# Kernel tuning notes

Hardware: AMD Instinct MI355X
Metric: run time of the kernel (lower is better)

## Reference

```python
import jax, jax.numpy as jnp
import numpy as np

DIM = 4096
X_H_SCALE = 1.0
HAD_SCALE = 1.0 / np.sqrt(DIM)  # orthonormal FWHT normalization


def fwht(x):
    """Fast Walsh-Hadamard transform along the last axis (Sylvester order).
    x: [..., N] with N a power of 2. O(N log N) butterfly, fully vectorized
    over all leading dims; the loop is over the fixed log2(N) stages only.
    """
    n = x.shape[-1]
    stages = int(np.log2(n))
    assert 1 << stages == n, "last dim must be a power of 2"
    lead = x.shape[:-1]
    for i in range(stages):
        blk = 1 << i  # block size doubling each stage
        y = x.reshape(lead + (n // (2 * blk), 2, blk))
        a = y[..., 0, :]
        b = y[..., 1, :]
        x = jnp.concatenate([a + b, a - b], axis=-1).reshape(lead + (n,))
    return x


def setup_inputs() -> dict:
    key = jax.random.key(0)
    x = jax.random.normal(key, (4, 2048, DIM), dtype=jnp.float32)
    return {"x": x}


def reference(x):
    # forward: qx = FWHT(x) * (had_scale / x_H_scale)
    scale = jnp.asarray(HAD_SCALE / X_H_SCALE, dtype=x.dtype)
    return fwht(x) * scale
```

## Files before the change

### kernel.cpp

```cpp
#include <hip/hip_runtime.h>

#define DIM 4096
#define HAD_SCALE 0.015625f

__device__ __forceinline__ int swz(int a) {
    return a ^ (((a >> 6) & 7) << 2);
}

__device__ __forceinline__ void fwht16(float r[16]) {
#pragma unroll
    for (int s = 1; s < 16; s <<= 1) {
#pragma unroll
        for (int i = 0; i < 16; i++) {
            if ((i & s) == 0) {
                float a = r[i];
                float b = r[i ^ s];
                r[i]     = a + b;
                r[i ^ s] = a - b;
            }
        }
    }
}

__global__ __launch_bounds__(256) void fwht_kernel(const float* __restrict__ x,
                                                   float* __restrict__ y) {
    __shared__ float lds[DIM];
    const int t = threadIdx.x;
    const size_t row = blockIdx.x;
    const float* xin = x + row * DIM;
    float* yout = y + row * DIM;

    float r[16];

    const float4* __restrict__ x4 = (const float4*)xin;
#pragma unroll
    for (int c = 0; c < 4; c++) {
        float4 v = x4[c * 256 + t];
        r[4 * c + 0] = v.x;
        r[4 * c + 1] = v.y;
        r[4 * c + 2] = v.z;
        r[4 * c + 3] = v.w;
    }
    fwht16(r);

#pragma unroll
    for (int c = 0; c < 4; c++) {
        int a = swz(4 * t + 1024 * c);
        *(float4*)&lds[a] = make_float4(r[4 * c + 0], r[4 * c + 1],
                                        r[4 * c + 2], r[4 * c + 3]);
    }
    __syncthreads();

    const int baseB = (t & 3) + ((t >> 2) << 6);
#pragma unroll
    for (int m = 0; m < 16; m++) r[m] = lds[swz(baseB + (m << 2))];
    fwht16(r);
#pragma unroll
    for (int m = 0; m < 16; m++) lds[swz(baseB + (m << 2))] = r[m];
    __syncthreads();

    const int baseC = (t & 63) + ((t >> 6) << 10);
#pragma unroll
    for (int m = 0; m < 16; m++) r[m] = lds[swz(baseC + (m << 6))];
    fwht16(r);

#pragma unroll
    for (int m = 0; m < 16; m++) yout[baseC + (m << 6)] = r[m] * HAD_SCALE;
}

extern "C" void kernel_launch(void* const* d_in, const int* in_sizes, int n_in,
                              void* d_out, int out_size, void* d_ws, size_t ws_size,
                              hipStream_t stream) {
    const float* x = (const float*)d_in[0];
    float* y = (float*)d_out;
    const int n = in_sizes[0];
    const int rows = n / DIM;
    fwht_kernel<<<rows, 256, 0, stream>>>(x, y);
}
```

Before: 225.6 us.

## Use one wave per row with 64-point register FWHT and single LDS pass

Restructures the 4096-point transform so each 64-thread block does two 64-point in-register butterfly stages with a single LDS exchange, instead of three 16-point stages with two exchanges across 256 threads. This removes one LDS round trip and one barrier. In exchange, register pressure rises sharply (64 floats per thread) and the final global stores become strided 4-byte writes rather than coalesced contiguous ones, which may hurt memory efficiency and occupancy.

After: 247.5 us. 1.1x slower.

```diff
diff --git a/kernel.cpp b/kernel.cpp
--- a/kernel.cpp
+++ b/kernel.cpp
@@ -4,14 +4,14 @@
 #define HAD_SCALE 0.015625f
 
 __device__ __forceinline__ int swz(int a) {
-    return a ^ (((a >> 6) & 7) << 2);
+    return a ^ (((a >> 8) & 7) << 2);
 }
 
-__device__ __forceinline__ void fwht16(float r[16]) {
+__device__ __forceinline__ void fwht64(float* r) {
 #pragma unroll
-    for (int s = 1; s < 16; s <<= 1) {
+    for (int s = 1; s < 64; s <<= 1) {
 #pragma unroll
-        for (int i = 0; i < 16; i++) {
+        for (int i = 0; i < 64; i++) {
             if ((i & s) == 0) {
                 float a = r[i];
                 float b = r[i ^ s];
@@ -22,50 +22,62 @@
     }
 }
 
-__global__ __launch_bounds__(256) void fwht_kernel(const float* __restrict__ x,
-                                                   float* __restrict__ y) {
+__global__ __launch_bounds__(64, 4) void fwht_kernel(const float* __restrict__ x,
+                                                     float* __restrict__ y) {
     __shared__ float lds[DIM];
-    const int t = threadIdx.x;
+    const int L = threadIdx.x;
     const size_t row = blockIdx.x;
     const float* xin = x + row * DIM;
     float* yout = y + row * DIM;
 
-    float r[16];
+    float4 r4[16];
+    float* r = (float*)r4;
 
     const float4* __restrict__ x4 = (const float4*)xin;
 #pragma unroll
-    for (int c = 0; c < 4; c++) {
-        float4 v = x4[c * 256 + t];
-        r[4 * c + 0] = v.x;
-        r[4 * c + 1] = v.y;
-        r[4 * c + 2] = v.z;
-        r[4 * c + 3] = v.w;
-    }
-    fwht16(r);
+    for (int c = 0; c < 16; c++) r4[c] = x4[c * 64 + L];
 
 #pragma unroll
-    for (int c = 0; c < 4; c++) {
-        int a = swz(4 * t + 1024 * c);
-        *(float4*)&lds[a] = make_float4(r[4 * c + 0], r[4 * c + 1],
-                                        r[4 * c + 2], r[4 * c + 3]);
+    for (int c = 0; c < 16; c++) {
+        float a0 = r[4 * c + 0], a1 = r[4 * c + 1];
+        float a2 = r[4 * c + 2], a3 = r[4 * c + 3];
+        float b0 = a0 + a1, b1 = a0 - a1, b2 = a2 + a3, b3 = a2 - a3;
+        r[4 * c + 0] = b0 + b2;
+        r[4 * c + 1] = b1 + b3;
+        r[4 * c + 2] = b0 - b2;
+        r[4 * c + 3] = b1 - b3;
+    }
+#pragma unroll
+    for (int s = 4; s < 64; s <<= 1) {
+#pragma unroll
+        for (int i = 0; i < 64; i++) {
+            if ((i & s) == 0) {
+                float a = r[i];
+                float b = r[i ^ s];
+                r[i]     = a + b;
+                r[i ^ s] = a - b;
+            }
+        }
+    }
+
+#pragma unroll
+    for (int c = 0; c < 16; c++) {
+        *(float4*)&lds[swz(4 * L + 256 * c)] = r4[c];
     }
     __syncthreads();
 
-    const int baseB = (t & 3) + ((t >> 2) << 6);
+    const int e = L & 3;
+    const int k = L >> 2;
+    const int base = e + (k << 8);
 #pragma unroll
-    for (int m = 0; m < 16; m++) r[m] = lds[swz(baseB + (m << 2))];
-    fwht16(r);
-#pragma unroll
-    for (int m = 0; m < 16; m++) lds[swz(baseB + (m << 2))] = r[m];
-    __syncthreads();
+    for (int v = 0; v < 64; v++) r[v] = lds[swz(base + (v << 2))];
 
-    const int baseC = (t & 63) + ((t >> 6) << 10);
-#pragma unroll
-    for (int m = 0; m < 16; m++) r[m] = lds[swz(baseC + (m << 6))];
-    fwht16(r);
+    fwht64(r);
 
 #pragma unroll
-    for (int m = 0; m < 16; m++) yout[baseC + (m << 6)] = r[m] * HAD_SCALE;
+    for (int v = 0; v < 64; v++) {
+        yout[base + (v << 2)] = r[v] * HAD_SCALE;
+    }
 }
 
 extern "C" void kernel_launch(void* const* d_in, const int* in_sizes, int n_in,
@@ -75,5 +87,5 @@
     float* y = (float*)d_out;
     const int n = in_sizes[0];
     const int rows = n / DIM;
-    fwht_kernel<<<rows, 256, 0, stream>>>(x, y);
+    fwht_kernel<<<rows, 64, 0, stream>>>(x, y);
 }
```
